# Kernel tuning notes

Hardware: AMD Instinct MI355X
Metric: run time of the kernel (lower is better)

## Reference

```python
import jax, jax.numpy as jnp
import numpy as np

SEG = 20  # patch size


def setup_inputs() -> dict:
    key = jax.random.key(0)
    k1, k2, k3, k4 = jax.random.split(key, 4)
    x = jax.random.uniform(k1, (2, 20, 1, 240, 240), dtype=jnp.float32)  # pixels in [0,1)
    emb_weight = jax.random.normal(k2, (256, 256), dtype=jnp.float32)
    pos_weight = jax.random.normal(k3, (144, 256), dtype=jnp.float32)
    temp_weight = jax.random.normal(k4, (20, 256), dtype=jnp.float32)
    return {"x": x, "emb_weight": emb_weight, "pos_weight": pos_weight, "temp_weight": temp_weight}


def reference(x, emb_weight, pos_weight, temp_weight):
    B, F, C, H, W = x.shape
    hp, wp = H // SEG, W // SEG  # 12, 12 -> 144 patches
    # segment_image: patches ordered row-major over (y, x), each patch flattened as [C, 20, 20]
    patches = x.reshape(B, F, C, hp, SEG, wp, SEG)
    patches = patches.transpose(0, 1, 3, 5, 2, 4, 6).reshape(B, F, hp * wp, C * SEG * SEG)
    idx = (patches * 255.0).astype(jnp.int32)          # truncation, matches .int()
    emb = emb_weight[idx].mean(axis=3)                 # [B, F, 144, 256] mean over pixels in patch
    emb = emb + pos_weight[None, None]                 # positional add
    cls = jnp.zeros((B, F, 1, emb.shape[-1]), emb.dtype)
    out = jnp.concatenate([cls, emb], axis=2)          # [B, F, 145, 256]
    out = out + temp_weight[:F][None, :, None, :]      # temporal add (incl. cls slot)
    return out
```

## Files before the change

kernel.cpp:

```cpp
#include <hip/hip_runtime.h>


#define F_   20
#define HW   240
#define SEG  20
#define PPB  12
#define BPF  12
#define NBLK (40 * BPF)
#define STRIP (HW * SEG)

typedef __attribute__((ext_vector_type(4))) float float4_t;

__device__ __forceinline__ float bits_f32(uint u) {
    union { uint i; float f; } c; c.i = u; return c.f;
}
__device__ __forceinline__ float bf16_to_f32(ushort u) { return bits_f32(((uint)u) << 16); }
__device__ __forceinline__ ushort f32_to_bf16(float v) {
    union { float f; uint i; } c; c.f = v;
    uint u = c.i;
    u += 0x7FFFu + ((u >> 16) & 1u);
    return (ushort)(u >> 16);
}

template<bool F32> __device__ __forceinline__ float4_t load4(const void* p, int i) {
    if constexpr (F32) {
        return *(const float4_t*)((const float*)p + i);
    } else {
        ushort4 u = *(const ushort4*)((const ushort*)p + i);
        float4_t r;
        r.x = bf16_to_f32(u.x); r.y = bf16_to_f32(u.y);
        r.z = bf16_to_f32(u.z); r.w = bf16_to_f32(u.w);
        return r;
    }
}
template<bool F32> __device__ __forceinline__ float load1(const void* p, int i) {
    if constexpr (F32) return ((const float*)p)[i];
    else               return bf16_to_f32(((const ushort*)p)[i]);
}
template<bool F32> __device__ __forceinline__ void store1(void* p, int i, float v) {
    if constexpr (F32) ((float*)p)[i] = v;
    else               ((ushort*)p)[i] = f32_to_bf16(v);
}

template<bool F32>
__device__ __forceinline__ void embed_body(
    const void* __restrict__ xg, const void* __restrict__ embg,
    const void* __restrict__ posg, const void* __restrict__ tempg,
    void* __restrict__ outg,
    float (&cntf)[PPB][256], float (&part)[PPB][4][256])
{
    const int tid  = threadIdx.x;
    const int lane = tid & 63;
    const int wave = tid >> 6;
    const int bf   = blockIdx.x / BPF;
    const int pr   = blockIdx.x % BPF;
    const int p0   = pr * 12;
    const int f    = bf % F_;

    const int xbase = bf * (HW * HW) + pr * STRIP;
    for (int it = 0; it < 5; ++it) {
        int i = tid + it * 256;
        if (i < STRIP / 4) {
            int elem = i * 4;
            int col  = elem % HW;
            int p    = col / SEG;
            float4_t v = load4<F32>(xg, xbase + elem);
            #pragma unroll
            for (int j = 0; j < 4; ++j) {
                int idx = (int)(v[j] * 255.0f);
                idx = idx < 0 ? 0 : (idx > 255 ? 255 : idx);
                atomicAdd(&cntf[p][idx], 1.0f);
            }
        }
    }
    __syncthreads();

    const int n0 = lane * 4;
    const int kbase = wave * 64;
    float acc[PPB][4];
    #pragma unroll
    for (int m = 0; m < PPB; ++m)
        #pragma unroll
        for (int c = 0; c < 4; ++c) acc[m][c] = 0.0f;

    #pragma unroll 2
    for (int kq = 0; kq < 16; ++kq) {
        const int k = kbase + kq * 4;
        float e[4][4];
        #pragma unroll
        for (int kk = 0; kk < 4; ++kk) {
            if constexpr (F32) {
                *(float4_t*)(&e[kk][0]) =
                    *(const float4_t*)((const float*)embg + (k + kk) * 256 + n0);
            } else {
                uint2 u = *(const uint2*)((const ushort*)embg + (k + kk) * 256 + n0);
                e[kk][0] = bits_f32(u.x << 16);
                e[kk][1] = bits_f32(u.x & 0xFFFF0000u);
                e[kk][2] = bits_f32(u.y << 16);
                e[kk][3] = bits_f32(u.y & 0xFFFF0000u);
            }
        }
        #pragma unroll
        for (int m = 0; m < PPB; ++m) {
            float4_t c4 = *(const float4_t*)(&cntf[m][k]);
            #pragma unroll
            for (int kk = 0; kk < 4; ++kk)
                #pragma unroll
                for (int c = 0; c < 4; ++c)
                    acc[m][c] += c4[kk] * e[kk][c];
        }
    }

    #pragma unroll
    for (int m = 0; m < PPB; ++m)
        *(float4_t*)(&part[m][wave][n0]) = *(float4_t*)(&acc[m][0]);
    __syncthreads();

    const int obase = bf * (145 * 256);
    const float tadd = load1<F32>(tempg, f * 256 + tid);
    if (pr == 0)
        store1<F32>(outg, obase + tid, tadd);
    #pragma unroll
    for (int m = 0; m < PPB; ++m) {
        float s = part[m][0][tid] + part[m][1][tid] + part[m][2][tid] + part[m][3][tid];
        int gp = p0 + m;
        float val = s * (1.0f / 400.0f) + load1<F32>(posg, gp * 256 + tid) + tadd;
        store1<F32>(outg, obase + (1 + gp) * 256 + tid, val);
    }
}

__global__ __launch_bounds__(256) void video_embed_v5_kernel(
    const void* __restrict__ xg, const void* __restrict__ embg,
    const void* __restrict__ posg, const void* __restrict__ tempg,
    void* __restrict__ outg)
{
    __shared__ float cntf[PPB][256];
    __shared__ float part[PPB][4][256];
    __shared__ int   isf32_s;

    const int tid = threadIdx.x;
    if (tid == 0) isf32_s = 0;
    __syncthreads();

    #pragma unroll
    for (int i = 0; i < PPB; ++i) cntf[i][tid] = 0.0f;
    if (tid < 128 && ((const ushort*)xg)[2 * tid] > 0x3F80u) isf32_s = 1;
    __syncthreads();

    if (isf32_s) embed_body<true >(xg, embg, posg, tempg, outg, cntf, part);
    else         embed_body<false>(xg, embg, posg, tempg, outg, cntf, part);
}

extern "C" void kernel_launch(void* const* d_in, const int* in_sizes, int n_in,
                              void* d_out, int out_size, void* d_ws, size_t ws_size,
                              hipStream_t stream) {
    video_embed_v5_kernel<<<dim3(NBLK), dim3(256), 0, stream>>>(
        d_in[0], d_in[1], d_in[2], d_in[3], d_out);
}
```

Before: 91.75 us.

## Use bf16 MFMA for histogram-times-embedding product with pre-transposed bf16 table

Adds a small prep kernel that transposes the embedding table into a bf16 copy in workspace. The main kernel then converts the per-patch pixel-value histograms to bf16 and computes histogram times embedding with 16x16x32 bf16 MFMA instructions, replacing the scalar FMA loop and the cross-wave shared-memory reduction. This targets the ALU cost of the matmul stage. In exchange it adds a second launch, rounds counts and weights to bf16 (counts up to 400 per bin round in bf16), and does less coalesced output stores.

```diff
diff --git a/kernel.cpp b/kernel.cpp
--- a/kernel.cpp
+++ b/kernel.cpp
@@ -10,6 +10,7 @@
 #define STRIP (HW * SEG)
 
 typedef __attribute__((ext_vector_type(4))) float float4_t;
+typedef __attribute__((ext_vector_type(8))) short short8_t;
 
 __device__ __forceinline__ float bits_f32(uint u) {
     union { uint i; float f; } c; c.i = u; return c.f;
@@ -43,11 +44,47 @@
 }
 
 template<bool F32>
+__device__ __forceinline__ void prep_body(const void* __restrict__ embg,
+                                          ushort* __restrict__ embT,
+                                          float (&tile)[64][65])
+{
+    const int tid = threadIdx.x;
+    const int tk  = blockIdx.x & 3;
+    const int tn  = blockIdx.x >> 2;
+    #pragma unroll
+    for (int i = 0; i < 16; ++i) {
+        int idx = tid + i * 256, r = idx >> 6, c = idx & 63;
+        tile[r][c] = load1<F32>(embg, (tk * 64 + r) * 256 + tn * 64 + c);
+    }
+    __syncthreads();
+    #pragma unroll
+    for (int i = 0; i < 16; ++i) {
+        int idx = tid + i * 256, r = idx >> 6, c = idx & 63;
+        embT[(tn * 64 + r) * 256 + tk * 64 + c] = f32_to_bf16(tile[c][r]);
+    }
+}
+
+__global__ __launch_bounds__(256) void video_embed_prep_v6(
+    const void* __restrict__ xg, const void* __restrict__ embg,
+    ushort* __restrict__ embT)
+{
+    __shared__ float tile[64][65];
+    __shared__ int isf32_s;
+    const int tid = threadIdx.x;
+    if (tid == 0) isf32_s = 0;
+    __syncthreads();
+    if (tid < 128 && ((const ushort*)xg)[2 * tid] > 0x3F80u) isf32_s = 1;
+    __syncthreads();
+    if (isf32_s) prep_body<true >(embg, embT, tile);
+    else         prep_body<false>(embg, embT, tile);
+}
+
+template<bool F32>
 __device__ __forceinline__ void embed_body(
-    const void* __restrict__ xg, const void* __restrict__ embg,
+    const void* __restrict__ xg, const ushort* __restrict__ embT,
     const void* __restrict__ posg, const void* __restrict__ tempg,
     void* __restrict__ outg,
-    float (&cntf)[PPB][256], float (&part)[PPB][4][256])
+    float (&cntf)[PPB][256], ushort (&cntb)[16][264])
 {
     const int tid  = threadIdx.x;
     const int lane = tid & 63;
@@ -75,85 +112,78 @@
     }
     __syncthreads();
 
-    const int n0 = lane * 4;
-    const int kbase = wave * 64;
-    float acc[PPB][4];
+    {
+        const int m  = tid >> 4;
+        const int c0 = (tid & 15) * 16;
+        #pragma unroll
+        for (int j = 0; j < 16; ++j) {
+            float v = (m < PPB) ? cntf[m][c0 + j] : 0.0f;
+            cntb[m][c0 + j] = f32_to_bf16(v);
+        }
+    }
+    __syncthreads();
+
+    const int am    = lane & 15;
+    const int quad  = lane >> 4;
+    const int wbase = wave * 64;
+    float4_t acc[4] = {{0,0,0,0},{0,0,0,0},{0,0,0,0},{0,0,0,0}};
     #pragma unroll
-    for (int m = 0; m < PPB; ++m)
+    for (int s = 0; s < 8; ++s) {
+        short8_t a = *(const short8_t*)(&cntb[am][s * 32 + quad * 8]);
         #pragma unroll
-        for (int c = 0; c < 4; ++c) acc[m][c] = 0.0f;
-
-    #pragma unroll 2
-    for (int kq = 0; kq < 16; ++kq) {
-        const int k = kbase + kq * 4;
-        float e[4][4];
-        #pragma unroll
-        for (int kk = 0; kk < 4; ++kk) {
-            if constexpr (F32) {
-                *(float4_t*)(&e[kk][0]) =
-                    *(const float4_t*)((const float*)embg + (k + kk) * 256 + n0);
-            } else {
-                uint2 u = *(const uint2*)((const ushort*)embg + (k + kk) * 256 + n0);
-                e[kk][0] = bits_f32(u.x << 16);
-                e[kk][1] = bits_f32(u.x & 0xFFFF0000u);
-                e[kk][2] = bits_f32(u.y << 16);
-                e[kk][3] = bits_f32(u.y & 0xFFFF0000u);
-            }
-        }
-        #pragma unroll
-        for (int m = 0; m < PPB; ++m) {
-            float4_t c4 = *(const float4_t*)(&cntf[m][k]);
-            #pragma unroll
-            for (int kk = 0; kk < 4; ++kk)
-                #pragma unroll
-                for (int c = 0; c < 4; ++c)
-                    acc[m][c] += c4[kk] * e[kk][c];
+        for (int t = 0; t < 4; ++t) {
+            short8_t b = *(const short8_t*)(embT + (wbase + t * 16 + am) * 256
+                                                 + s * 32 + quad * 8);
+            acc[t] = __builtin_amdgcn_mfma_f32_16x16x32_bf16(a, b, acc[t], 0, 0, 0);
         }
     }
 
+    const int obase = bf * (145 * 256);
+    if (pr == 0)
+        store1<F32>(outg, obase + tid, load1<F32>(tempg, f * 256 + tid));
     #pragma unroll
-    for (int m = 0; m < PPB; ++m)
-        *(float4_t*)(&part[m][wave][n0]) = *(float4_t*)(&acc[m][0]);
-    __syncthreads();
-
-    const int obase = bf * (145 * 256);
-    const float tadd = load1<F32>(tempg, f * 256 + tid);
-    if (pr == 0)
-        store1<F32>(outg, obase + tid, tadd);
-    #pragma unroll
-    for (int m = 0; m < PPB; ++m) {
-        float s = part[m][0][tid] + part[m][1][tid] + part[m][2][tid] + part[m][3][tid];
-        int gp = p0 + m;
-        float val = s * (1.0f / 400.0f) + load1<F32>(posg, gp * 256 + tid) + tadd;
-        store1<F32>(outg, obase + (1 + gp) * 256 + tid, val);
+    for (int t = 0; t < 4; ++t) {
+        #pragma unroll
+        for (int r = 0; r < 4; ++r) {
+            int m = quad * 4 + r;
+            if (m < PPB) {
+                int gp = p0 + m;
+                int n  = wbase + t * 16 + am;
+                float val = acc[t][r] * (1.0f / 400.0f)
+                          + load1<F32>(posg, gp * 256 + n)
+                          + load1<F32>(tempg, f * 256 + n);
+                store1<F32>(outg, obase + (1 + gp) * 256 + n, val);
+            }
+        }
     }
 }
 
-__global__ __launch_bounds__(256) void video_embed_v5_kernel(
-    const void* __restrict__ xg, const void* __restrict__ embg,
+__global__ __launch_bounds__(256) void video_embed_v6_kernel(
+    const void* __restrict__ xg, const ushort* __restrict__ embT,
     const void* __restrict__ posg, const void* __restrict__ tempg,
     void* __restrict__ outg)
 {
     __shared__ float cntf[PPB][256];
-    __shared__ float part[PPB][4][256];
-    __shared__ int   isf32_s;
+    __shared__ __align__(16) ushort cntb[16][264];
+    __shared__ int isf32_s;
 
     const int tid = threadIdx.x;
     if (tid == 0) isf32_s = 0;
     __syncthreads();
-
     #pragma unroll
     for (int i = 0; i < PPB; ++i) cntf[i][tid] = 0.0f;
     if (tid < 128 && ((const ushort*)xg)[2 * tid] > 0x3F80u) isf32_s = 1;
     __syncthreads();
 
-    if (isf32_s) embed_body<true >(xg, embg, posg, tempg, outg, cntf, part);
-    else         embed_body<false>(xg, embg, posg, tempg, outg, cntf, part);
+    if (isf32_s) embed_body<true >(xg, embT, posg, tempg, outg, cntf, cntb);
+    else         embed_body<false>(xg, embT, posg, tempg, outg, cntf, cntb);
 }
 
 extern "C" void kernel_launch(void* const* d_in, const int* in_sizes, int n_in,
                               void* d_out, int out_size, void* d_ws, size_t ws_size,
                               hipStream_t stream) {
-    video_embed_v5_kernel<<<dim3(NBLK), dim3(256), 0, stream>>>(
-        d_in[0], d_in[1], d_in[2], d_in[3], d_out);
+    ushort* embT = (ushort*)d_ws;
+    video_embed_prep_v6<<<dim3(16), dim3(256), 0, stream>>>(d_in[0], d_in[1], embT);
+    video_embed_v6_kernel<<<dim3(NBLK), dim3(256), 0, stream>>>(
+        d_in[0], embT, d_in[2], d_in[3], d_out);
 }
```

New measurement: 86.92 us. 1.06x faster.
